# Performance work log

Hardware: AMD Instinct MI355X
Metric: run time of the kernel (lower is better)

The kernel has to match this reference:

```python
import jax, jax.numpy as jnp
import numpy as np
from jax import lax

B, N, F_IN, T = 4, 30000, 2, 12
HID, HORIZON, E = 32, 12, 240000


def setup_inputs() -> dict:
    key = jax.random.key(0)
    ks = jax.random.split(key, 20)

    def lin_init(k, fan_in, shape):
        b = 1.0 / np.sqrt(fan_in)
        return jax.random.uniform(k, shape, jnp.float32, -b, b)

    def glorot(k, shape):
        b = np.sqrt(6.0 / (shape[0] + shape[1]))
        return jax.random.uniform(k, shape, jnp.float32, -b, b)

    return {
        "x": jax.random.normal(ks[0], (B, N, F_IN, T), jnp.float32),
        "edge_index": jax.random.randint(ks[1], (2, E), 0, N, jnp.int32),
        # A3TGCN2 attention over periods (init: uniform[0,1))
        "attention": jax.random.uniform(ks[2], (T,), jnp.float32),
        # TGCN2 gates: GCNConv weight (F_IN,HID) + bias, Linear (2*HID,HID) + bias
        "conv_z_w": glorot(ks[3], (F_IN, HID)), "conv_z_b": jnp.zeros((HID,), jnp.float32),
        "lin_z_w": lin_init(ks[4], 2 * HID, (2 * HID, HID)), "lin_z_b": lin_init(ks[5], 2 * HID, (HID,)),
        "conv_r_w": glorot(ks[6], (F_IN, HID)), "conv_r_b": jnp.zeros((HID,), jnp.float32),
        "lin_r_w": lin_init(ks[7], 2 * HID, (2 * HID, HID)), "lin_r_b": lin_init(ks[8], 2 * HID, (HID,)),
        "conv_h_w": glorot(ks[9], (F_IN, HID)), "conv_h_b": jnp.zeros((HID,), jnp.float32),
        "lin_h_w": lin_init(ks[10], 2 * HID, (2 * HID, HID)), "lin_h_b": lin_init(ks[11], 2 * HID, (HID,)),
        # trailing head Linear(HID, HORIZON)
        "head_w": lin_init(ks[12], HID, (HID, HORIZON)), "head_b": lin_init(ks[13], HID, (HORIZON,)),
    }


def _forward(x, attention, conv_z_w, conv_z_b, lin_z_w, lin_z_b,
             conv_r_w, conv_r_b, lin_r_w, lin_r_b,
             conv_h_w, conv_h_b, lin_h_w, lin_h_b,
             head_w, head_b, edge_index):
    b, n = x.shape[0], x.shape[1]
    # GCN normalization with added self loops: D^-1/2 (A+I) D^-1/2
    loop = jnp.arange(n, dtype=edge_index.dtype)
    src = jnp.concatenate([edge_index[0], loop])  # (E+N,) message sources
    dst = jnp.concatenate([edge_index[1], loop])  # (E+N,) message targets
    deg = jnp.zeros((n,), x.dtype).at[dst].add(1.0)  # deg >= 1 due to self loops
    dinv = lax.rsqrt(deg)
    norm = dinv[src] * dinv[dst]  # (E+N,)

    def gcn(xt, W, bias):
        # xt: (B,N,F) -> (B,N,HID); gather from src, scatter-add to dst
        xw = jnp.einsum('bnf,fh->bnh', xt, W)
        msg = xw[:, src, :] * norm[None, :, None]  # (B,E+N,HID)
        agg = jnp.zeros((b, n, W.shape[1]), xt.dtype).at[:, dst, :].add(msg)
        return agg + bias

    probs = jax.nn.softmax(attention)  # (T,)
    H0 = jnp.zeros((b, n, HID), x.dtype)  # A3TGCN2 passes H=None every period

    def step(acc, inps):
        xt, p = inps  # xt: (B,N,F)
        Z = jax.nn.sigmoid(jnp.concatenate([gcn(xt, conv_z_w, conv_z_b), H0], -1) @ lin_z_w + lin_z_b)
        R = jax.nn.sigmoid(jnp.concatenate([gcn(xt, conv_r_w, conv_r_b), H0], -1) @ lin_r_w + lin_r_b)
        Ht = jnp.tanh(jnp.concatenate([gcn(xt, conv_h_w, conv_h_b), H0 * R], -1) @ lin_h_w + lin_h_b)
        Hn = Z * H0 + (1.0 - Z) * Ht
        return acc + p * Hn, None

    acc, _ = lax.scan(step, H0, (jnp.moveaxis(x, 3, 0), probs))
    return jax.nn.relu(acc) @ head_w + head_b  # (B,N,HORIZON)


def reference(x, edge_index, attention, conv_z_w, conv_z_b, lin_z_w, lin_z_b,
              conv_r_w, conv_r_b, lin_r_w, lin_r_b,
              conv_h_w, conv_h_b, lin_h_w, lin_h_b, head_w, head_b):
    return _forward(x, attention, conv_z_w, conv_z_b, lin_z_w, lin_z_b,
                    conv_r_w, conv_r_b, lin_r_w, lin_r_b,
                    conv_h_w, conv_h_b, lin_h_w, lin_h_b,
                    head_w, head_b, edge_index)
```

## Files before the change

kernel.cpp:

```cpp
#include <hip/hip_runtime.h>

#define BB   4
#define NN   30000
#define TT   12
#define EE   240000
#define FT   24
#define NM   96
#define CAP  32
#define OVCAP 2048
#define TRB  (NN * NM / 256)
#define FB   ((EE + 255) / 256)

#define WS_CNT 0
#define WS_OVC 30000
#define WS_EFF 30016
#define WS_OVF 30272
#define WS_BKT 34368
#define WS_XT  994368

__global__ void __launch_bounds__(256)
k_pre(const float* __restrict__ x, const int* __restrict__ src,
      const int* __restrict__ dst,
      const float* __restrict__ czw, const float* __restrict__ czb,
      const float* __restrict__ lzw, const float* __restrict__ lzb,
      const float* __restrict__ chw, const float* __restrict__ chb,
      const float* __restrict__ lhw, const float* __restrict__ lhb,
      const float* __restrict__ att,
      float* __restrict__ xt, int* __restrict__ cnt, int* __restrict__ ovc,
      int* __restrict__ ovf, int* __restrict__ bucket, float* __restrict__ eff) {
    int bid = blockIdx.x, lt = threadIdx.x;
    if (bid < TRB) {
        int tid = bid * 256 + lt;
        int n = tid / NM, c = tid - NM * n;
        int b = c / FT, ft = c - FT * b;
        xt[tid] = x[(b * NN + n) * FT + ft];
        return;
    }
    if (bid < TRB + FB) {
        int e = (bid - TRB) * 256 + lt;
        if (e < EE) {
            int d = dst[e], s = src[e];
            int slot = atomicAdd(&cnt[d], 1);
            if (slot < CAP) {
                bucket[d * CAP + slot] = s;
            } else {
                int o = atomicAdd(ovc, 1);
                if (o < OVCAP) { ovf[2 * o] = d; ovf[2 * o + 1] = s; }
            }
        }
        return;
    }
    int j = lt;
    if (j < 32) {
        float wz0 = 0.f, wz1 = 0.f, bz = 0.f, wh0 = 0.f, wh1 = 0.f, bh = 0.f;
        for (int k = 0; k < 32; ++k) {
            float lz = lzw[k * 32 + j], lh = lhw[k * 32 + j];
            wz0 = fmaf(czw[k],      lz, wz0);
            wz1 = fmaf(czw[32 + k], lz, wz1);
            bz  = fmaf(czb[k],      lz, bz);
            wh0 = fmaf(chw[k],      lh, wh0);
            wh1 = fmaf(chw[32 + k], lh, wh1);
            bh  = fmaf(chb[k],      lh, bh);
        }
        eff[j]        = wz0;
        eff[32 + j]   = wz1;
        eff[64 + j]   = bz + lzb[j];
        eff[96 + j]   = wh0;
        eff[128 + j]  = wh1;
        eff[160 + j]  = bh + lhb[j];
    } else if (j == 32) {
        float m = -1e30f;
        for (int t = 0; t < TT; ++t) m = fmaxf(m, att[t]);
        float p[TT], s = 0.f;
        for (int t = 0; t < TT; ++t) { p[t] = __expf(att[t] - m); s += p[t]; }
        float inv = 1.0f / s;
        for (int t = 0; t < TT; ++t) eff[192 + t] = p[t] * inv;
    }
}

__global__ void __launch_bounds__(256)
k_fused(const float* __restrict__ xt, const int* __restrict__ cnt,
        const int* __restrict__ ovc, const int* __restrict__ ovf,
        const int* __restrict__ bucket, const float* __restrict__ eff,
        const float* __restrict__ hw, const float* __restrict__ hb,
        float* __restrict__ out) {
    __shared__ float se[204];
    __shared__ float shw[384];
    __shared__ float shb[12];
    __shared__ float sx[4 * NM];
    __shared__ float lacc[4 * 132];
    const int lt = threadIdx.x, lane = lt & 63, w = lt >> 6;
    const int n = blockIdx.x * 4 + w;

    if (lt < 204) se[lt] = eff[lt];
    if (lt >= 204 && lt < 216) shb[lt - 204] = hb[lt - 204];
    shw[lt] = hw[lt];
    if (lt < 128) shw[256 + lt] = hw[256 + lt];
    __syncthreads();

    const int deg = __builtin_amdgcn_readfirstlane(cnt[n]);
    const float dn = rsqrtf((float)(deg + 1));
    const bool act = (lane < 48);

    float2 acc = {0.f, 0.f};
    {
        const float2* rn = (const float2*)(xt + (long long)n * NM);
        if (act) { float2 v = rn[lane]; acc.x = dn * v.x; acc.y = dn * v.y; }
    }

    const int m = (deg < CAP) ? deg : CAP;
    const int* brow = bucket + n * CAP;
    int k = 0;
    for (; k + 4 <= m; k += 4) {
        int s0 = __builtin_amdgcn_readfirstlane(brow[k]);
        int s1 = __builtin_amdgcn_readfirstlane(brow[k + 1]);
        int s2 = __builtin_amdgcn_readfirstlane(brow[k + 2]);
        int s3 = __builtin_amdgcn_readfirstlane(brow[k + 3]);
        int c0 = __builtin_amdgcn_readfirstlane(cnt[s0]);
        int c1 = __builtin_amdgcn_readfirstlane(cnt[s1]);
        int c2 = __builtin_amdgcn_readfirstlane(cnt[s2]);
        int c3 = __builtin_amdgcn_readfirstlane(cnt[s3]);
        const float2* r0 = (const float2*)(xt + (long long)s0 * NM);
        const float2* r1 = (const float2*)(xt + (long long)s1 * NM);
        const float2* r2 = (const float2*)(xt + (long long)s2 * NM);
        const float2* r3 = (const float2*)(xt + (long long)s3 * NM);
        float w0 = rsqrtf((float)(c0 + 1));
        float w1 = rsqrtf((float)(c1 + 1));
        float w2 = rsqrtf((float)(c2 + 1));
        float w3 = rsqrtf((float)(c3 + 1));
        if (act) {
            float2 v0 = r0[lane], v1 = r1[lane], v2 = r2[lane], v3 = r3[lane];
            acc.x = fmaf(w0, v0.x, acc.x); acc.y = fmaf(w0, v0.y, acc.y);
            acc.x = fmaf(w1, v1.x, acc.x); acc.y = fmaf(w1, v1.y, acc.y);
            acc.x = fmaf(w2, v2.x, acc.x); acc.y = fmaf(w2, v2.y, acc.y);
            acc.x = fmaf(w3, v3.x, acc.x); acc.y = fmaf(w3, v3.y, acc.y);
        }
    }
    for (; k < m; ++k) {
        int s = __builtin_amdgcn_readfirstlane(brow[k]);
        int cs = __builtin_amdgcn_readfirstlane(cnt[s]);
        const float2* rs = (const float2*)(xt + (long long)s * NM);
        float ws_ = rsqrtf((float)(cs + 1));
        if (act) {
            float2 v = rs[lane];
            acc.x = fmaf(ws_, v.x, acc.x); acc.y = fmaf(ws_, v.y, acc.y);
        }
    }

    int nov = __builtin_amdgcn_readfirstlane(*ovc);
    if (nov > OVCAP) nov = OVCAP;
    for (int i = 0; i < nov; ++i) {
        int d = ovf[2 * i];
        if (d == n) {
            int s = ovf[2 * i + 1];
            int cs = cnt[s];
            float ws_ = rsqrtf((float)(cs + 1));
            const float2* rs = (const float2*)(xt + (long long)s * NM);
            if (act) {
                float2 v = rs[lane];
                acc.x = fmaf(ws_, v.x, acc.x); acc.y = fmaf(ws_, v.y, acc.y);
            }
        }
    }

    if (act) {
        sx[w * NM + 2 * lane]     = dn * acc.x;
        sx[w * NM + 2 * lane + 1] = dn * acc.y;
    }
    __syncthreads();

    const int j = lane & 31, b0_ = lane >> 5;
    const float wz0 = se[j],      wz1 = se[32 + j],  bz = se[64 + j];
    const float wh0 = se[96 + j], wh1 = se[128 + j], bh = se[160 + j];
#pragma unroll
    for (int bi = 0; bi < 2; ++bi) {
        const int b = b0_ + 2 * bi;
        const float* srow = sx + w * NM + b * FT;
        float a = 0.f;
#pragma unroll
        for (int t = 0; t < TT; ++t) {
            float v0 = srow[t], v1 = srow[12 + t], p = se[192 + t];
            float zp = fmaf(v1, wz1, fmaf(v0, wz0, bz));
            float inv = __builtin_amdgcn_rcpf(1.0f + __expf(zp));
            float hp = fmaf(v1, wh1, fmaf(v0, wh0, bh));
            hp = fminf(fmaxf(hp + hp, -30.0f), 30.0f);
            float e2 = __expf(hp);
            float h  = (e2 - 1.0f) * __builtin_amdgcn_rcpf(e2 + 1.0f);
            a = fmaf(p * inv, h, a);
        }
        lacc[w * 132 + b * 33 + j] = fmaxf(a, 0.f);
    }
    __syncthreads();

    if (lane < 48) {
        int b = lane / 12, kk = lane - 12 * b;
        float r = shb[kk];
        const float* la = lacc + w * 132 + b * 33;
#pragma unroll
        for (int jj = 0; jj < 32; ++jj)
            r = fmaf(la[jj], shw[jj * 12 + kk], r);
        out[((long long)b * NN + n) * 12 + kk] = r;
    }
}

extern "C" void kernel_launch(void* const* d_in, const int* in_sizes, int n_in,
                              void* d_out, int out_size, void* d_ws, size_t ws_size,
                              hipStream_t stream) {
    const float* x   = (const float*)d_in[0];
    const int*   ei  = (const int*)d_in[1];
    const float* att = (const float*)d_in[2];
    const float* czw = (const float*)d_in[3];
    const float* czb = (const float*)d_in[4];
    const float* lzw = (const float*)d_in[5];
    const float* lzb = (const float*)d_in[6];
    const float* chw = (const float*)d_in[11];
    const float* chb = (const float*)d_in[12];
    const float* lhw = (const float*)d_in[13];
    const float* lhb = (const float*)d_in[14];
    const float* hw  = (const float*)d_in[15];
    const float* hb  = (const float*)d_in[16];
    float* out = (float*)d_out;

    float* ws = (float*)d_ws;
    int*   cnt = (int*)(ws + WS_CNT);
    int*   ovc = (int*)(ws + WS_OVC);
    float* eff = ws + WS_EFF;
    int*   ovf = (int*)(ws + WS_OVF);
    int*   bkt = (int*)(ws + WS_BKT);
    float* xt  = ws + WS_XT;

    const int* src = ei;
    const int* dst = ei + EE;

    hipMemsetAsync(cnt, 0, (WS_EFF) * 4, stream);
    k_pre<<<TRB + FB + 1, 256, 0, stream>>>(x, src, dst, czw, czb, lzw, lzb,
                                            chw, chb, lhw, lhb, att,
                                            xt, cnt, ovc, ovf, bkt, eff);
    k_fused<<<NN / 4, 256, 0, stream>>>(xt, cnt, ovc, ovf, bkt, eff, hw, hb, out);
}
```

Baseline: 152.1 us.

## Gather directly from input layout and preload neighbor indices via readlane

```diff
diff --git a/kernel.cpp b/kernel.cpp
--- a/kernel.cpp
+++ b/kernel.cpp
@@ -8,7 +8,6 @@
 #define NM   96
 #define CAP  32
 #define OVCAP 2048
-#define TRB  (NN * NM / 256)
 #define FB   ((EE + 255) / 256)
 
 #define WS_CNT 0
@@ -16,28 +15,23 @@
 #define WS_EFF 30016
 #define WS_OVF 30272
 #define WS_BKT 34368
-#define WS_XT  994368
+
+__device__ __forceinline__ float readlane_f(float v, int l) {
+    return __int_as_float(__builtin_amdgcn_readlane(__float_as_int(v), l));
+}
 
 __global__ void __launch_bounds__(256)
-k_pre(const float* __restrict__ x, const int* __restrict__ src,
-      const int* __restrict__ dst,
+k_pre(const int* __restrict__ src, const int* __restrict__ dst,
       const float* __restrict__ czw, const float* __restrict__ czb,
       const float* __restrict__ lzw, const float* __restrict__ lzb,
       const float* __restrict__ chw, const float* __restrict__ chb,
       const float* __restrict__ lhw, const float* __restrict__ lhb,
       const float* __restrict__ att,
-      float* __restrict__ xt, int* __restrict__ cnt, int* __restrict__ ovc,
+      int* __restrict__ cnt, int* __restrict__ ovc,
       int* __restrict__ ovf, int* __restrict__ bucket, float* __restrict__ eff) {
     int bid = blockIdx.x, lt = threadIdx.x;
-    if (bid < TRB) {
-        int tid = bid * 256 + lt;
-        int n = tid / NM, c = tid - NM * n;
-        int b = c / FT, ft = c - FT * b;
-        xt[tid] = x[(b * NN + n) * FT + ft];
-        return;
-    }
-    if (bid < TRB + FB) {
-        int e = (bid - TRB) * 256 + lt;
+    if (bid < FB) {
+        int e = bid * 256 + lt;
         if (e < EE) {
             int d = dst[e], s = src[e];
             int slot = atomicAdd(&cnt[d], 1);
@@ -79,7 +73,7 @@
 }
 
 __global__ void __launch_bounds__(256)
-k_fused(const float* __restrict__ xt, const int* __restrict__ cnt,
+k_fused(const float* __restrict__ x, const int* __restrict__ cnt,
         const int* __restrict__ ovc, const int* __restrict__ ovf,
         const int* __restrict__ bucket, const float* __restrict__ eff,
         const float* __restrict__ hw, const float* __restrict__ hb,
@@ -98,74 +92,60 @@
     if (lt < 128) shw[256 + lt] = hw[256 + lt];
     __syncthreads();
 
+    const bool act = (lane < 48);
+    const int b = lane / 12, f2 = lane - 12 * b;
+    const float2* xb = (const float2*)x;
+    const int lane_off = b * (NN * 12) + f2;
+
     const int deg = __builtin_amdgcn_readfirstlane(cnt[n]);
-    const float dn = rsqrtf((float)(deg + 1));
-    const bool act = (lane < 48);
+    const int m = (deg < CAP) ? deg : CAP;
+    int sv = (lane < m) ? bucket[n * CAP + lane] : n;
+    float wv = (lane <= m) ? rsqrtf((float)(cnt[sv] + 1)) : 0.f;
 
     float2 acc = {0.f, 0.f};
-    {
-        const float2* rn = (const float2*)(xt + (long long)n * NM);
-        if (act) { float2 v = rn[lane]; acc.x = dn * v.x; acc.y = dn * v.y; }
-    }
-
-    const int m = (deg < CAP) ? deg : CAP;
-    const int* brow = bucket + n * CAP;
-    int k = 0;
-    for (; k + 4 <= m; k += 4) {
-        int s0 = __builtin_amdgcn_readfirstlane(brow[k]);
-        int s1 = __builtin_amdgcn_readfirstlane(brow[k + 1]);
-        int s2 = __builtin_amdgcn_readfirstlane(brow[k + 2]);
-        int s3 = __builtin_amdgcn_readfirstlane(brow[k + 3]);
-        int c0 = __builtin_amdgcn_readfirstlane(cnt[s0]);
-        int c1 = __builtin_amdgcn_readfirstlane(cnt[s1]);
-        int c2 = __builtin_amdgcn_readfirstlane(cnt[s2]);
-        int c3 = __builtin_amdgcn_readfirstlane(cnt[s3]);
-        const float2* r0 = (const float2*)(xt + (long long)s0 * NM);
-        const float2* r1 = (const float2*)(xt + (long long)s1 * NM);
-        const float2* r2 = (const float2*)(xt + (long long)s2 * NM);
-        const float2* r3 = (const float2*)(xt + (long long)s3 * NM);
-        float w0 = rsqrtf((float)(c0 + 1));
-        float w1 = rsqrtf((float)(c1 + 1));
-        float w2 = rsqrtf((float)(c2 + 1));
-        float w3 = rsqrtf((float)(c3 + 1));
+    const int mm4 = (m + 4) & ~3;
+    for (int k = 0; k < mm4; k += 4) {
+        int s0 = __builtin_amdgcn_readlane(sv, k);
+        int s1 = __builtin_amdgcn_readlane(sv, k + 1);
+        int s2 = __builtin_amdgcn_readlane(sv, k + 2);
+        int s3 = __builtin_amdgcn_readlane(sv, k + 3);
+        float w0 = readlane_f(wv, k);
+        float w1 = readlane_f(wv, k + 1);
+        float w2 = readlane_f(wv, k + 2);
+        float w3 = readlane_f(wv, k + 3);
         if (act) {
-            float2 v0 = r0[lane], v1 = r1[lane], v2 = r2[lane], v3 = r3[lane];
+            float2 v0 = xb[lane_off + s0 * 12];
+            float2 v1 = xb[lane_off + s1 * 12];
+            float2 v2 = xb[lane_off + s2 * 12];
+            float2 v3 = xb[lane_off + s3 * 12];
             acc.x = fmaf(w0, v0.x, acc.x); acc.y = fmaf(w0, v0.y, acc.y);
             acc.x = fmaf(w1, v1.x, acc.x); acc.y = fmaf(w1, v1.y, acc.y);
             acc.x = fmaf(w2, v2.x, acc.x); acc.y = fmaf(w2, v2.y, acc.y);
             acc.x = fmaf(w3, v3.x, acc.x); acc.y = fmaf(w3, v3.y, acc.y);
         }
     }
-    for (; k < m; ++k) {
-        int s = __builtin_amdgcn_readfirstlane(brow[k]);
-        int cs = __builtin_amdgcn_readfirstlane(cnt[s]);
-        const float2* rs = (const float2*)(xt + (long long)s * NM);
-        float ws_ = rsqrtf((float)(cs + 1));
-        if (act) {
-            float2 v = rs[lane];
-            acc.x = fmaf(ws_, v.x, acc.x); acc.y = fmaf(ws_, v.y, acc.y);
-        }
-    }
 
     int nov = __builtin_amdgcn_readfirstlane(*ovc);
-    if (nov > OVCAP) nov = OVCAP;
-    for (int i = 0; i < nov; ++i) {
-        int d = ovf[2 * i];
-        if (d == n) {
-            int s = ovf[2 * i + 1];
-            int cs = cnt[s];
-            float ws_ = rsqrtf((float)(cs + 1));
-            const float2* rs = (const float2*)(xt + (long long)s * NM);
-            if (act) {
-                float2 v = rs[lane];
-                acc.x = fmaf(ws_, v.x, acc.x); acc.y = fmaf(ws_, v.y, acc.y);
+    if (nov > 0) {
+        if (nov > OVCAP) nov = OVCAP;
+        for (int i = 0; i < nov; ++i) {
+            int d = ovf[2 * i];
+            if (d == n) {
+                int s = ovf[2 * i + 1];
+                float ws_ = rsqrtf((float)(cnt[s] + 1));
+                if (act) {
+                    float2 v = xb[lane_off + s * 12];
+                    acc.x = fmaf(ws_, v.x, acc.x);
+                    acc.y = fmaf(ws_, v.y, acc.y);
+                }
             }
         }
     }
 
+    const float dn = readlane_f(wv, m);
     if (act) {
-        sx[w * NM + 2 * lane]     = dn * acc.x;
-        sx[w * NM + 2 * lane + 1] = dn * acc.y;
+        sx[w * NM + b * FT + f2 * 2]     = dn * acc.x;
+        sx[w * NM + b * FT + f2 * 2 + 1] = dn * acc.y;
     }
     __syncthreads();
 
@@ -174,8 +154,8 @@
     const float wh0 = se[96 + j], wh1 = se[128 + j], bh = se[160 + j];
 #pragma unroll
     for (int bi = 0; bi < 2; ++bi) {
-        const int b = b0_ + 2 * bi;
-        const float* srow = sx + w * NM + b * FT;
+        const int bb = b0_ + 2 * bi;
+        const float* srow = sx + w * NM + bb * FT;
         float a = 0.f;
 #pragma unroll
         for (int t = 0; t < TT; ++t) {
@@ -188,18 +168,18 @@
             float h  = (e2 - 1.0f) * __builtin_amdgcn_rcpf(e2 + 1.0f);
             a = fmaf(p * inv, h, a);
         }
-        lacc[w * 132 + b * 33 + j] = fmaxf(a, 0.f);
+        lacc[w * 132 + bb * 33 + j] = fmaxf(a, 0.f);
     }
     __syncthreads();
 
     if (lane < 48) {
-        int b = lane / 12, kk = lane - 12 * b;
+        int bb = lane / 12, kk = lane - 12 * bb;
         float r = shb[kk];
-        const float* la = lacc + w * 132 + b * 33;
+        const float* la = lacc + w * 132 + bb * 33;
 #pragma unroll
         for (int jj = 0; jj < 32; ++jj)
             r = fmaf(la[jj], shw[jj * 12 + kk], r);
-        out[((long long)b * NN + n) * 12 + kk] = r;
+        out[((long long)bb * NN + n) * 12 + kk] = r;
     }
 }
 
@@ -227,14 +207,13 @@
     float* eff = ws + WS_EFF;
     int*   ovf = (int*)(ws + WS_OVF);
     int*   bkt = (int*)(ws + WS_BKT);
-    float* xt  = ws + WS_XT;
 
     const int* src = ei;
     const int* dst = ei + EE;
 
-    hipMemsetAsync(cnt, 0, (WS_EFF) * 4, stream);
-    k_pre<<<TRB + FB + 1, 256, 0, stream>>>(x, src, dst, czw, czb, lzw, lzb,
-                                            chw, chb, lhw, lhb, att,
-                                            xt, cnt, ovc, ovf, bkt, eff);
-    k_fused<<<NN / 4, 256, 0, stream>>>(xt, cnt, ovc, ovf, bkt, eff, hw, hb, out);
-}
+    hipMemsetAsync(cnt, 0, WS_EFF * 4, stream);
+    k_pre<<<FB + 1, 256, 0, stream>>>(src, dst, czw, czb, lzw, lzb,
+                                      chw, chb, lhw, lhb, att,
+                                      cnt, ovc, ovf, bkt, eff);
+    k_fused<<<NN / 4, 256, 0, stream>>>(x, cnt, ovc, ovf, bkt, eff, hw, hb, out);
+}
```

After: 146.0 us. 4.0% less time.
